# Kernel tuning notes

Measured on AMD Instinct MI355X. Metric: run time of the kernel, lower is better.

## Reference

```python
import jax, jax.numpy as jnp
import numpy as np

TAU = 0.5
EPS = 1e-08


def setup_inputs() -> dict:
    key = jax.random.key(0)
    k1, k2 = jax.random.split(key)
    B, D = 8192, 128
    z_a = jax.random.normal(k1, (B, D), dtype=jnp.float32)
    z_b = jax.random.normal(k2, (B, D), dtype=jnp.float32)
    return {"z_a": z_a, "z_b": z_b}


def reference(z_a, z_b):
    B = z_a.shape[0]
    N = 2 * B
    z = jnp.concatenate([z_a, z_b], axis=0)           # [2B, D]
    sim = (z @ z.T) / TAU                             # [2B, 2B]
    sp = jax.nn.softplus(sim)
    # zero out self-similarity (diagonal)
    idx = jnp.arange(N)
    sp = sp.at[idx, idx].set(0.0)
    denom = jnp.maximum(sp.sum(axis=-1), EPS)         # [2B]
    pos_idx = (idx + B) % N
    sp_pos = sp[idx, pos_idx]                         # [2B]
    log_p = jnp.log(jnp.maximum(sp_pos, EPS)) - jnp.log(denom)
    return -log_p.mean()
```

## Files before the change

kernel.cpp:

```cpp
#include <hip/hip_runtime.h>
#include <hip/hip_bf16.h>

constexpr int Bh = 8192;
constexpr int Nn = 16384;
constexpr int Dd = 128;
constexpr float EPS = 1e-8f;
constexpr float LN2 = 0.69314718056f;

constexpr int K_TILES = 16;
constexpr int N_TILES = 16512;
constexpr int N_BLOCKS = N_TILES / K_TILES;

typedef short bf16x8 __attribute__((ext_vector_type(8)));
typedef float f32x4 __attribute__((ext_vector_type(4)));

__global__ __launch_bounds__(256) void convert_kernel(const float4* __restrict__ za,
                                                      const float4* __restrict__ zb,
                                                      ushort* __restrict__ z,
                                                      float* __restrict__ rowsum,
                                                      int* __restrict__ counter,
                                                      float* __restrict__ possum) {
    const int t = blockIdx.x * 256 + threadIdx.x;
    constexpr int Q = (Bh * Dd) / 4;
    const float SCL = 1.69864363f;
    float4 v = (t < Q) ? za[t] : zb[t - Q];
    union { ushort4 u4; __hip_bfloat16 h[4]; } cv;
    cv.h[0] = __float2bfloat16(v.x * SCL);
    cv.h[1] = __float2bfloat16(v.y * SCL);
    cv.h[2] = __float2bfloat16(v.z * SCL);
    cv.h[3] = __float2bfloat16(v.w * SCL);
    ((ushort4*)z)[t] = cv.u4;
    if (t < Nn) rowsum[t] = 0.f;
    if (t == 0) { counter[0] = 0; possum[0] = 0.f; }
}

__device__ __forceinline__ int row_tile_of(int g) {
    int t = (int)((257.0f - sqrtf((float)(66049 - 4 * g))) * 0.5f);
    t = t < 0 ? 0 : (t > 127 ? 127 : t);
    while (t * (257 - t) > g) --t;
    while ((t + 1) * (256 - t) <= g) ++t;
    return t;
}

__device__ __forceinline__ void flush_rs(float* __restrict__ rowsum, int rowW,
                                         float (&rs)[2][4], int q, int c) {
#pragma unroll
    for (int s = 0; s < 2; ++s)
#pragma unroll
        for (int r = 0; r < 4; ++r) {
            float v = rs[s][r];
            v += __shfl_xor(v, 1);
            v += __shfl_xor(v, 2);
            v += __shfl_xor(v, 4);
            v += __shfl_xor(v, 8);
            if (c == 0) atomicAdd(&rowsum[rowW + s * 16 + q * 4 + r], v);
            rs[s][r] = 0.f;
        }
}

__device__ __forceinline__ void colflush(float* __restrict__ rowsum,
                                         float (&csumP)[4], int C0P, int lane, int c) {
#pragma unroll
    for (int st = 0; st < 4; ++st) {
        float v = csumP[st];
        v += __shfl_xor(v, 16);
        v += __shfl_xor(v, 32);
        if (lane < 16) atomicAdd(&rowsum[C0P + st * 16 + c], v);
    }
}

__device__ __forceinline__ void stage_tile(const ushort* __restrict__ z, ushort* lbuf,
                                           int C0, int wave, int lane) {
#pragma unroll
    for (int i = 0; i < 4; ++i) {
        const int chunk = wave * 4 + i;
        const int r = (chunk << 2) + (lane >> 4);
        const int bl = ((lane & 15) ^ (r & 15)) << 4;
        const char* gp = (const char*)z + (((size_t)(C0 + r)) << 8) + bl;
        ushort* lp = lbuf + (chunk << 9);
        __builtin_amdgcn_global_load_lds((const __attribute__((address_space(1))) void*)gp,
                                         (__attribute__((address_space(3))) void*)lp,
                                         16, 0, 0);
    }
}

__global__ __launch_bounds__(256) void main_kernel(const ushort* __restrict__ z,
                                                   float* __restrict__ rowsum,
                                                   int* __restrict__ counter,
                                                   float* __restrict__ possum,
                                                   float* __restrict__ out) {
    __shared__ ushort ldsb[2][8192];

    const int tid = threadIdx.x;
    const int wave = tid >> 6;
    const int lane = tid & 63;
    const int q = lane >> 4;
    const int c = lane & 15;
    const int g0 = blockIdx.x * K_TILES;

    int tr = row_tile_of(g0);
    int ct = 2 * tr + (g0 - tr * (257 - tr));

    int O[4];
#pragma unroll
    for (int kt = 0; kt < 4; ++kt) O[kt] = (c << 8) + ((((q + 4 * kt) ^ c)) << 4);

    bf16x8 afrag[2][4];
    float rs[2][4];
#pragma unroll
    for (int s = 0; s < 2; ++s)
#pragma unroll
        for (int r = 0; r < 4; ++r) rs[s][r] = 0.f;

    const f32x4 Z4 = {0.f, 0.f, 0.f, 0.f};

    float pacc = 0.f;
    float csumP[4];
    int C0P = 0;
    bool pendP = false;
    int cur_tr = -1, rowW = 0, cur = 0;

    stage_tile(z, &ldsb[0][0], ct << 6, wave, lane);
    __syncthreads();

    for (int j = 0; j < K_TILES; ++j) {
        const int C0 = ct << 6;
        const bool diag = ((ct >> 1) == tr);

        if (tr != cur_tr) {
            if (cur_tr >= 0) flush_rs(rowsum, rowW, rs, q, c);
            cur_tr = tr;
            rowW = (tr << 7) + wave * 32;
#pragma unroll
            for (int s = 0; s < 2; ++s) {
                const ushort* ap = z + (size_t)(rowW + s * 16 + c) * Dd;
#pragma unroll
                for (int kt = 0; kt < 4; ++kt)
                    afrag[s][kt] = *(const bf16x8*)(ap + kt * 32 + q * 8);
            }
        }

        if (pendP) { colflush(rowsum, csumP, C0P, lane, c); pendP = false; }

        int trN = tr, ctN = ct + 1;
        if (ctN == 256) { trN = tr + 1; ctN = 2 * trN; }
        if (j + 1 < K_TILES) stage_tile(z, &ldsb[cur ^ 1][0], ctN << 6, wave, lane);

        const char* lb = (const char*)&ldsb[cur][0];
        float csum[4];
#pragma unroll
        for (int st = 0; st < 4; ++st) csum[st] = 0.f;

        f32x4 acc[2][2];
#pragma unroll
        for (int st = 0; st < 5; ++st) {
            const int p = st & 1;
            if (st < 4) {
                bf16x8 bcur[4];
#pragma unroll
                for (int kt = 0; kt < 4; ++kt)
                    bcur[kt] = *(const bf16x8*)(lb + O[kt] + st * 4096);
#pragma unroll
                for (int s = 0; s < 2; ++s)
                    acc[p][s] = __builtin_amdgcn_mfma_f32_16x16x32_bf16(afrag[s][0], bcur[0], Z4, 0, 0, 0);
#pragma unroll
                for (int kt = 1; kt < 4; ++kt) {
#pragma unroll
                    for (int s = 0; s < 2; ++s)
                        acc[p][s] = __builtin_amdgcn_mfma_f32_16x16x32_bf16(afrag[s][kt], bcur[kt], acc[p][s], 0, 0, 0);
                }
            }
            if (st > 0) {
                const int stP = st - 1;
                const int pp = p ^ 1;
                const int gc0 = C0 + stP * 16;
#pragma unroll
                for (int s = 0; s < 2; ++s) {
                    const int R = rowW + s * 16;
                    float sp[4];
#pragma unroll
                    for (int r = 0; r < 4; ++r) {
                        float u = acc[pp][s][r];
                        float e = __builtin_amdgcn_exp2f(-fabsf(u));
                        sp[r] = fmaxf(u, 0.f) + __builtin_amdgcn_logf(1.f + e);
                    }
                    if (diag && gc0 == R) {
#pragma unroll
                        for (int r = 0; r < 4; ++r)
                            if (c == q * 4 + r) sp[r] = 0.f;
                    }
                    if (gc0 == (R ^ Bh)) {
#pragma unroll
                        for (int r = 0; r < 4; ++r)
                            if (c == q * 4 + r)
                                pacc += __logf(fmaxf(LN2 * sp[r], EPS));
                    }
#pragma unroll
                    for (int r = 0; r < 4; ++r) rs[s][r] += sp[r];
                    if (!diag) csum[stP] += (sp[0] + sp[1]) + (sp[2] + sp[3]);
                }
            }
        }

        if (!diag) {
#pragma unroll
            for (int st = 0; st < 4; ++st) csumP[st] = csum[st];
            C0P = C0;
            pendP = true;
        }

        __syncthreads();
        cur ^= 1;
        tr = trN;
        ct = ctN;
    }

    if (pendP) colflush(rowsum, csumP, C0P, lane, c);
    if (cur_tr >= 0) flush_rs(rowsum, rowW, rs, q, c);

    {
        float v = pacc;
#pragma unroll
        for (int m = 1; m < 64; m <<= 1) v += __shfl_xor(v, m);
        if (lane == 0 && v != 0.f) atomicAdd(possum, v + v);
    }

    __syncthreads();
    int* shi = (int*)&ldsb[0][0];
    if (tid == 0) shi[0] = atomicAdd(counter, 1);
    __syncthreads();
    if (shi[0] == N_BLOCKS - 1) {
        float acc = 0.f;
#pragma unroll
        for (int b = 0; b < 8; ++b) {
            float v[8];
#pragma unroll
            for (int k = 0; k < 8; ++k)
                v[k] = __hip_atomic_load(&rowsum[tid + (b * 8 + k) * 256],
                                         __ATOMIC_RELAXED, __HIP_MEMORY_SCOPE_AGENT);
#pragma unroll
            for (int k = 0; k < 8; ++k)
                acc += __logf(fmaxf(LN2 * v[k], EPS));
        }
#pragma unroll
        for (int m = 1; m < 64; m <<= 1) acc += __shfl_xor(acc, m);
        __syncthreads();
        float* red = (float*)&ldsb[0][0];
        if (lane == 0) red[wave] = acc;
        __syncthreads();
        if (tid == 0) {
            float ps = __hip_atomic_load(possum, __ATOMIC_RELAXED, __HIP_MEMORY_SCOPE_AGENT);
            float sumden = red[0] + red[1] + red[2] + red[3];
            out[0] = (sumden - ps) / (float)Nn;
        }
    }
}

extern "C" void kernel_launch(void* const* d_in, const int* in_sizes, int n_in,
                              void* d_out, int out_size, void* d_ws, size_t ws_size,
                              hipStream_t stream) {
    const float* za = (const float*)d_in[0];
    const float* zb = (const float*)d_in[1];

    ushort* z = (ushort*)d_ws;
    float* rowsum = (float*)((char*)d_ws + (size_t)Nn * Dd * 2);
    int* counter = (int*)(rowsum + Nn);
    float* possum = (float*)(rowsum + Nn + 32);
    float* out = (float*)d_out;

    convert_kernel<<<2048, 256, 0, stream>>>((const float4*)za, (const float4*)zb, z, rowsum, counter, possum);
    main_kernel<<<N_BLOCKS, 256, 0, stream>>>(z, rowsum, counter, possum, out);
}
```

Baseline: 167.1 us.

## Split each tile's columns across two waves with 512-thread blocks and halve tiles per block

```diff
diff --git a/kernel.cpp b/kernel.cpp
--- a/kernel.cpp
+++ b/kernel.cpp
@@ -7,7 +7,7 @@
 constexpr float EPS = 1e-8f;
 constexpr float LN2 = 0.69314718056f;
 
-constexpr int K_TILES = 16;
+constexpr int K_TILES = 8;
 constexpr int N_TILES = 16512;
 constexpr int N_BLOCKS = N_TILES / K_TILES;
 
@@ -59,21 +59,21 @@
 }
 
 __device__ __forceinline__ void colflush(float* __restrict__ rowsum,
-                                         float (&csumP)[4], int C0P, int lane, int c) {
-#pragma unroll
-    for (int st = 0; st < 4; ++st) {
+                                         float (&csumP)[2], int base, int lane, int c) {
+#pragma unroll
+    for (int st = 0; st < 2; ++st) {
         float v = csumP[st];
         v += __shfl_xor(v, 16);
         v += __shfl_xor(v, 32);
-        if (lane < 16) atomicAdd(&rowsum[C0P + st * 16 + c], v);
+        if (lane < 16) atomicAdd(&rowsum[base + st * 16 + c], v);
     }
 }
 
 __device__ __forceinline__ void stage_tile(const ushort* __restrict__ z, ushort* lbuf,
                                            int C0, int wave, int lane) {
 #pragma unroll
-    for (int i = 0; i < 4; ++i) {
-        const int chunk = wave * 4 + i;
+    for (int i = 0; i < 2; ++i) {
+        const int chunk = wave * 2 + i;
         const int r = (chunk << 2) + (lane >> 4);
         const int bl = ((lane & 15) ^ (r & 15)) << 4;
         const char* gp = (const char*)z + (((size_t)(C0 + r)) << 8) + bl;
@@ -84,7 +84,7 @@
     }
 }
 
-__global__ __launch_bounds__(256) void main_kernel(const ushort* __restrict__ z,
+__global__ __launch_bounds__(512) void main_kernel(const ushort* __restrict__ z,
                                                    float* __restrict__ rowsum,
                                                    int* __restrict__ counter,
                                                    float* __restrict__ possum,
@@ -93,6 +93,8 @@
 
     const int tid = threadIdx.x;
     const int wave = tid >> 6;
+    const int wr = wave >> 1;
+    const int cg = wave & 1;
     const int lane = tid & 63;
     const int q = lane >> 4;
     const int c = lane & 15;
@@ -115,8 +117,8 @@
     const f32x4 Z4 = {0.f, 0.f, 0.f, 0.f};
 
     float pacc = 0.f;
-    float csumP[4];
-    int C0P = 0;
+    float csumP[2];
+    int baseP = 0;
     bool pendP = false;
     int cur_tr = -1, rowW = 0, cur = 0;
 
@@ -130,7 +132,7 @@
         if (tr != cur_tr) {
             if (cur_tr >= 0) flush_rs(rowsum, rowW, rs, q, c);
             cur_tr = tr;
-            rowW = (tr << 7) + wave * 32;
+            rowW = (tr << 7) + wr * 32;
 #pragma unroll
             for (int s = 0; s < 2; ++s) {
                 const ushort* ap = z + (size_t)(rowW + s * 16 + c) * Dd;
@@ -140,26 +142,25 @@
             }
         }
 
-        if (pendP) { colflush(rowsum, csumP, C0P, lane, c); pendP = false; }
+        if (pendP) { colflush(rowsum, csumP, baseP, lane, c); pendP = false; }
 
         int trN = tr, ctN = ct + 1;
         if (ctN == 256) { trN = tr + 1; ctN = 2 * trN; }
         if (j + 1 < K_TILES) stage_tile(z, &ldsb[cur ^ 1][0], ctN << 6, wave, lane);
 
         const char* lb = (const char*)&ldsb[cur][0];
-        float csum[4];
-#pragma unroll
-        for (int st = 0; st < 4; ++st) csum[st] = 0.f;
+        float csum[2] = {0.f, 0.f};
 
         f32x4 acc[2][2];
 #pragma unroll
-        for (int st = 0; st < 5; ++st) {
+        for (int st = 0; st < 3; ++st) {
             const int p = st & 1;
-            if (st < 4) {
+            if (st < 2) {
+                const int stG = cg * 2 + st;
                 bf16x8 bcur[4];
 #pragma unroll
                 for (int kt = 0; kt < 4; ++kt)
-                    bcur[kt] = *(const bf16x8*)(lb + O[kt] + st * 4096);
+                    bcur[kt] = *(const bf16x8*)(lb + O[kt] + stG * 4096);
 #pragma unroll
                 for (int s = 0; s < 2; ++s)
                     acc[p][s] = __builtin_amdgcn_mfma_f32_16x16x32_bf16(afrag[s][0], bcur[0], Z4, 0, 0, 0);
@@ -173,7 +174,7 @@
             if (st > 0) {
                 const int stP = st - 1;
                 const int pp = p ^ 1;
-                const int gc0 = C0 + stP * 16;
+                const int gc0 = C0 + (cg * 2 + stP) * 16;
 #pragma unroll
                 for (int s = 0; s < 2; ++s) {
                     const int R = rowW + s * 16;
@@ -203,9 +204,9 @@
         }
 
         if (!diag) {
-#pragma unroll
-            for (int st = 0; st < 4; ++st) csumP[st] = csum[st];
-            C0P = C0;
+            csumP[0] = csum[0];
+            csumP[1] = csum[1];
+            baseP = C0 + cg * 32;
             pendP = true;
         }
 
@@ -215,7 +216,7 @@
         ct = ctN;
     }
 
-    if (pendP) colflush(rowsum, csumP, C0P, lane, c);
+    if (pendP) colflush(rowsum, csumP, baseP, lane, c);
     if (cur_tr >= 0) flush_rs(rowsum, rowW, rs, q, c);
 
     {
@@ -232,11 +233,11 @@
     if (shi[0] == N_BLOCKS - 1) {
         float acc = 0.f;
 #pragma unroll
-        for (int b = 0; b < 8; ++b) {
+        for (int b = 0; b < 4; ++b) {
             float v[8];
 #pragma unroll
             for (int k = 0; k < 8; ++k)
-                v[k] = __hip_atomic_load(&rowsum[tid + (b * 8 + k) * 256],
+                v[k] = __hip_atomic_load(&rowsum[tid + (b * 8 + k) * 512],
                                          __ATOMIC_RELAXED, __HIP_MEMORY_SCOPE_AGENT);
 #pragma unroll
             for (int k = 0; k < 8; ++k)
@@ -250,7 +251,8 @@
         __syncthreads();
         if (tid == 0) {
             float ps = __hip_atomic_load(possum, __ATOMIC_RELAXED, __HIP_MEMORY_SCOPE_AGENT);
-            float sumden = red[0] + red[1] + red[2] + red[3];
+            float sumden = red[0] + red[1] + red[2] + red[3]
+                         + red[4] + red[5] + red[6] + red[7];
             out[0] = (sumden - ps) / (float)Nn;
         }
     }
@@ -269,5 +271,5 @@
     float* out = (float*)d_out;
 
     convert_kernel<<<2048, 256, 0, stream>>>((const float4*)za, (const float4*)zb, z, rowsum, counter, possum);
-    main_kernel<<<N_BLOCKS, 256, 0, stream>>>(z, rowsum, counter, possum, out);
-}
+    main_kernel<<<N_BLOCKS, 512, 0, stream>>>(z, rowsum, counter, possum, out);
+}
```

After: 172.9 us. +3.5%, slower.
